# Optimization experiments

Measured on AMD Instinct MI355X. Metric: run time of the kernel, lower is better.

The kernel has to match this reference:

```python
import jax, jax.numpy as jnp
import numpy as np

ALPHA = 10.0
BETA = 2.0
BASE = 0.5
N, D, N_CLASSES = 4096, 512, 128


def setup_inputs() -> dict:
    key = jax.random.key(0)
    k1, k2 = jax.random.split(key)
    x = jax.random.normal(k1, (N, D), dtype=jnp.float32)
    inputs = x / jnp.linalg.norm(x, axis=1, keepdims=True)  # L2-normalized embeddings
    targets = jax.random.randint(k2, (N,), 0, N_CLASSES, dtype=jnp.int64)
    margin = jnp.float32(0.5)
    return {"inputs": inputs, "targets": targets, "margin": margin}


def reference(inputs, targets, margin):
    # Vectorized equivalent of the per-row masked_select/sort/hard-mining loop.
    n = inputs.shape[0]
    sim = inputs @ inputs.T  # [n, n]
    same = targets[:, None] == targets[None, :]
    pos_mask = same & (sim < 1.0)        # positives, excluding self-sim == 1
    neg_mask = ~same

    # sort()[0] / sort()[-1]  ==  masked min / max
    min_pos = jnp.min(jnp.where(pos_mask, sim, jnp.inf), axis=1)    # pos_pair_[0]
    max_neg = jnp.max(jnp.where(neg_mask, sim, -jnp.inf), axis=1)   # neg_pair_[-1]

    # Hard mining: selected values equal the raw sims (the +/- margin and
    # min_pos/max_neg shifts cancel algebraically in the original code).
    sel_neg = neg_mask & (sim + margin - min_pos[:, None] > 0)
    sel_pos = pos_mask & (max_neg[:, None] - sim + margin > 0)

    pos_sum = jnp.sum(jnp.where(sel_pos, jnp.exp(-BETA * (sim - BASE)), 0.0), axis=1)
    neg_sum = jnp.sum(jnp.where(sel_neg, jnp.exp(ALPHA * (sim - BASE)), 0.0), axis=1)
    row_loss = (2.0 / BETA) * jnp.log1p(pos_sum) + (2.0 / ALPHA) * jnp.log1p(neg_sum)

    # Rows with no surviving pos or neg pairs are skipped (counted in c).
    valid = jnp.any(sel_pos, axis=1) & jnp.any(sel_neg, axis=1)
    loss = jnp.sum(jnp.where(valid, row_loss, 0.0)) / n
    prec = jnp.mean((~valid).astype(jnp.float32))

    # Original returns mean sims of the LAST row's (pre-mining) pos/neg pairs.
    lp = pos_mask[-1].astype(sim.dtype)
    ln = neg_mask[-1].astype(sim.dtype)
    mean_pos_sim = jnp.sum(sim[-1] * lp) / jnp.maximum(jnp.sum(lp), 1.0)
    mean_neg_sim = jnp.sum(sim[-1] * ln) / jnp.maximum(jnp.sum(ln), 1.0)
    return (loss, prec, mean_pos_sim, mean_neg_sim)
```

## Files before the change

### kernel.cpp

```cpp
#include <hip/hip_runtime.h>
#include <hip/hip_bf16.h>
#include <math.h>

#define NROWS 4096
#define DDIM  512
#define BM    128
#define BK    128
#define NT    (DDIM / BK)
#define NBLK  (NROWS / BM)
#define NTRI  (NBLK * (NBLK + 1) / 2)

static constexpr float ALPHA = 10.0f;
static constexpr float BETA  = 2.0f;
static constexpr float BASE  = 0.5f;

typedef short bf16x8 __attribute__((ext_vector_type(8)));
typedef float f32x4 __attribute__((ext_vector_type(4)));

__device__ __forceinline__ unsigned f2bf(float f) {
  __hip_bfloat16 h = __float2bfloat16(f);
  return (unsigned)*reinterpret_cast<unsigned short*>(&h);
}
__device__ __forceinline__ float bf2f(unsigned short u) {
  return __uint_as_float(((unsigned)u) << 16);
}

#define GLOAD_LDS16(g, l)                                              \
  __builtin_amdgcn_global_load_lds(                                    \
      (const __attribute__((address_space(1))) void*)(g),              \
      (__attribute__((address_space(3))) void*)(l), 16, 0, 0)

__global__ __launch_bounds__(256) void convert_k(const float* __restrict__ X,
                                                 unsigned short* __restrict__ Xb) {
  const int wid = threadIdx.x >> 6, lane = threadIdx.x & 63;
  const int r = blockIdx.x * 4 + wid;
  const size_t base = (size_t)r * DDIM + lane * 8;
  const float4 v0 = *reinterpret_cast<const float4*>(X + base);
  const float4 v1 = *reinterpret_cast<const float4*>(X + base + 4);
  uint4 u;
  u.x = f2bf(v0.x) | (f2bf(v0.y) << 16);
  u.y = f2bf(v0.z) | (f2bf(v0.w) << 16);
  u.z = f2bf(v1.x) | (f2bf(v1.y) << 16);
  u.w = f2bf(v1.z) | (f2bf(v1.w) << 16);
  *reinterpret_cast<uint4*>(Xb + base) = u;
}

__global__ __launch_bounds__(256) void gemm_tri_store(
    const unsigned short* __restrict__ Xb, unsigned short* __restrict__ simb) {
  __shared__ unsigned short lds[2][BM * BK] __attribute__((aligned(16)));

  const int bswz = (blockIdx.x & 7) * (NTRI / 8) + (blockIdx.x >> 3);
  int kk0 = bswz, bi = 0;
  while (kk0 >= NBLK - bi) { kk0 -= NBLK - bi; ++bi; }
  const int bj = bi + kk0;
  const int i0 = bi * BM, j0 = bj * BM;
  const bool diagb = (bi == bj);

  const int tid = threadIdx.x;
  const int w = tid >> 6, lane = tid & 63;
  const int wr = w >> 1, wc = w & 1;
  const int g = lane >> 4, q = lane & 15;
  const char* Xbb = (const char*)Xb;

  f32x4 acc[4][4];
  #pragma unroll
  for (int m = 0; m < 4; ++m)
    #pragma unroll
    for (int n = 0; n < 4; ++n) acc[m][n] = (f32x4)0.0f;

  for (int t = 0; t < NT; ++t) {
    {
      const int kb = t * (BK * 2);
      #pragma unroll
      for (int c = 0; c < 8; ++c) {
        const int lin = (c * 256 + tid) * 16;
        const int row = lin >> 8;
        const int col = lin & 255;
        const int scol = col ^ ((row & 15) << 4);
        GLOAD_LDS16(Xbb + (size_t)(i0 + row) * (DDIM * 2) + kb + scol,
                    (char*)&lds[0][0] + lin);
        if (!diagb)
          GLOAD_LDS16(Xbb + (size_t)(j0 + row) * (DDIM * 2) + kb + scol,
                      (char*)&lds[1][0] + lin);
      }
    }
    __syncthreads();
    const char* Ab = (const char*)&lds[0][0];
    const char* Bb = diagb ? Ab : (const char*)&lds[1][0];
    #pragma unroll
    for (int kk = 0; kk < 4; ++kk) {
      bf16x8 a[4], b[4];
      #pragma unroll
      for (int fm = 0; fm < 4; ++fm) {
        const int row = wr * 64 + fm * 16 + q;
        const int colb = (kk * 64 + g * 16) ^ ((row & 15) << 4);
        a[fm] = *reinterpret_cast<const bf16x8*>(Ab + row * 256 + colb);
      }
      #pragma unroll
      for (int fn = 0; fn < 4; ++fn) {
        const int row = wc * 64 + fn * 16 + q;
        const int colb = (kk * 64 + g * 16) ^ ((row & 15) << 4);
        b[fn] = *reinterpret_cast<const bf16x8*>(Bb + row * 256 + colb);
      }
      #pragma unroll
      for (int fm = 0; fm < 4; ++fm)
        #pragma unroll
        for (int fn = 0; fn < 4; ++fn)
          acc[fm][fn] = __builtin_amdgcn_mfma_f32_16x16x32_bf16(a[fm], b[fn], acc[fm][fn], 0, 0, 0);
    }
    __syncthreads();
  }

  unsigned short* SV = &lds[0][0];

  #pragma unroll
  for (int fm = 0; fm < 4; ++fm)
    #pragma unroll
    for (int reg = 0; reg < 4; ++reg) {
      const int rloc = wr * 64 + fm * 16 + g * 4 + reg;
      #pragma unroll
      for (int fn = 0; fn < 4; ++fn) {
        const int cloc = wc * 64 + fn * 16 + q;
        unsigned short v = (unsigned short)f2bf(acc[fm][fn][reg]);
        if (diagb && rloc == cloc) v = 0x3F80;
        SV[rloc * 136 + cloc] = v;
      }
    }
  __syncthreads();
  #pragma unroll
  for (int rr = 0; rr < 8; ++rr) {
    const int s = rr * 256 + tid;
    const int row = s >> 4, cs = s & 15;
    const bf16x8 vv = *reinterpret_cast<const bf16x8*>(&SV[row * 136 + cs * 8]);
    *reinterpret_cast<bf16x8*>(simb + (size_t)(i0 + row) * NROWS + j0 + cs * 8) = vv;
  }

  if (!diagb) {
    __syncthreads();
    #pragma unroll
    for (int fn = 0; fn < 4; ++fn) {
      const int shrow = wc * 64 + fn * 16 + q;
      #pragma unroll
      for (int fm = 0; fm < 4; ++fm) {
        const int colR = wr * 64 + fm * 16 + g * 4;
        uint2 uu;
        uu.x = f2bf(acc[fm][fn][0]) | (f2bf(acc[fm][fn][1]) << 16);
        uu.y = f2bf(acc[fm][fn][2]) | (f2bf(acc[fm][fn][3]) << 16);
        *reinterpret_cast<uint2*>(&SV[shrow * 136 + colR]) = uu;
      }
    }
    __syncthreads();
    #pragma unroll
    for (int rr = 0; rr < 8; ++rr) {
      const int s = rr * 256 + tid;
      const int row = s >> 4, cs = s & 15;
      const bf16x8 vv = *reinterpret_cast<const bf16x8*>(&SV[row * 136 + cs * 8]);
      *reinterpret_cast<bf16x8*>(simb + (size_t)(j0 + row) * NROWS + i0 + cs * 8) = vv;
    }
  }
}

__global__ __launch_bounds__(256) void rows_k(
    const unsigned short* __restrict__ simb, const int* __restrict__ tgt,
    const float* __restrict__ marginp, float* __restrict__ rowloss,
    float* __restrict__ rowvalid, float* __restrict__ lacc) {
  __shared__ int tgl[NROWS];
  const int tid = threadIdx.x;
  #pragma unroll
  for (int c = 0; c < 4; ++c)
    reinterpret_cast<int4*>(tgl)[tid + c * 256] =
        reinterpret_cast<const int4*>(tgt)[tid + c * 256];
  __syncthreads();

  const int wid = tid >> 6, lane = tid & 63;
  const int i = blockIdx.x * 4 + wid;
  const int ti = tgl[i];
  const unsigned short* row = simb + (size_t)i * NROWS;
  const bool lastw = (i == NROWS - 1);

  bf16x8 v[8];
  unsigned long long same = 0ull;
  float minp = INFINITY, maxn = -INFINITY;
  #pragma unroll
  for (int c = 0; c < 8; ++c) {
    const int j0 = c * 512 + lane * 8;
    v[c] = *reinterpret_cast<const bf16x8*>(row + j0);
    const int4 t0 = *reinterpret_cast<const int4*>(tgl + j0);
    const int4 t1 = *reinterpret_cast<const int4*>(tgl + j0 + 4);
    const int tj[8] = {t0.x, t0.y, t0.z, t0.w, t1.x, t1.y, t1.z, t1.w};
    #pragma unroll
    for (int e = 0; e < 8; ++e) {
      const float s = bf2f((unsigned short)v[c][e]);
      const bool sm = (tj[e] == ti);
      same |= (unsigned long long)sm << (c * 8 + e);
      if (sm) {
        if (s < 1.0f) minp = fminf(minp, s);
      } else {
        maxn = fmaxf(maxn, s);
      }
    }
  }
  #pragma unroll
  for (int off = 1; off < 64; off <<= 1) {
    minp = fminf(minp, __shfl_xor(minp, off));
    maxn = fmaxf(maxn, __shfl_xor(maxn, off));
  }

  const float margin = *marginp;
  float psum = 0.0f, nsum = 0.0f;
  float lsp = 0.0f, lcp = 0.0f, lsn = 0.0f, lcn = 0.0f;
  #pragma unroll
  for (int c = 0; c < 8; ++c) {
    #pragma unroll
    for (int e = 0; e < 8; ++e) {
      const float s = bf2f((unsigned short)v[c][e]);
      const bool sm = (same >> (c * 8 + e)) & 1ull;
      if (!sm) {
        if (s + margin - minp > 0.0f) nsum += __expf(ALPHA * (s - BASE));
        if (lastw) { lsn += s; lcn += 1.0f; }
      } else if (s < 1.0f) {
        if (maxn - s + margin > 0.0f) psum += __expf(-BETA * (s - BASE));
        if (lastw) { lsp += s; lcp += 1.0f; }
      }
    }
  }
  #pragma unroll
  for (int off = 1; off < 64; off <<= 1) {
    psum += __shfl_xor(psum, off);
    nsum += __shfl_xor(nsum, off);
  }
  if (lastw) {
    #pragma unroll
    for (int off = 1; off < 64; off <<= 1) {
      lsp += __shfl_xor(lsp, off); lcp += __shfl_xor(lcp, off);
      lsn += __shfl_xor(lsn, off); lcn += __shfl_xor(lcn, off);
    }
  }
  if (lane == 0) {
    const bool valid = (psum > 0.0f) && (nsum > 0.0f);
    rowloss[i] = valid ? (2.0f / BETA) * log1pf(psum) + (2.0f / ALPHA) * log1pf(nsum) : 0.0f;
    rowvalid[i] = valid ? 0.0f : 1.0f;
    if (lastw) { lacc[0] = lsp; lacc[1] = lcp; lacc[2] = lsn; lacc[3] = lcn; }
  }
}

__device__ __forceinline__ float block_sum(float v) {
  __shared__ float sh[4];
  #pragma unroll
  for (int off = 32; off > 0; off >>= 1) v += __shfl_down(v, off);
  if ((threadIdx.x & 63) == 0) sh[threadIdx.x >> 6] = v;
  __syncthreads();
  float r = sh[0] + sh[1] + sh[2] + sh[3];
  __syncthreads();
  return r;
}

__global__ __launch_bounds__(256) void finalize_k(
    const float* __restrict__ rowloss, const float* __restrict__ rowvalid,
    const float* __restrict__ lacc, float* __restrict__ out) {
  float lsum = 0.0f, inval = 0.0f;
  #pragma unroll
  for (int c = 0; c < 16; ++c) {
    const int i = c * 256 + threadIdx.x;
    lsum += rowloss[i];
    inval += rowvalid[i];
  }
  lsum = block_sum(lsum);
  inval = block_sum(inval);
  if (threadIdx.x == 0) {
    out[0] = lsum / (float)NROWS;
    out[1] = inval / (float)NROWS;
    out[2] = lacc[0] / fmaxf(lacc[1], 1.0f);
    out[3] = lacc[2] / fmaxf(lacc[3], 1.0f);
  }
}

extern "C" void kernel_launch(void* const* d_in, const int* in_sizes, int n_in,
                              void* d_out, int out_size, void* d_ws, size_t ws_size,
                              hipStream_t stream) {
  const float* X = (const float*)d_in[0];
  const int* tgt = (const int*)d_in[1];
  const float* marginp = (const float*)d_in[2];
  float* out = (float*)d_out;

  char* ws = (char*)d_ws;
  float* rowloss = (float*)ws;
  float* rowvalid = (float*)(ws + (16 << 10));
  float* lacc = (float*)(ws + (32 << 10));
  unsigned short* Xb = (unsigned short*)(ws + (128 << 10));
  unsigned short* simb = (unsigned short*)(ws + (128 << 10) + ((size_t)4 << 20));

  convert_k<<<dim3(NROWS / 4), 256, 0, stream>>>(X, Xb);
  gemm_tri_store<<<dim3(NTRI), 256, 0, stream>>>(Xb, simb);
  rows_k<<<dim3(NROWS / 4), 256, 0, stream>>>(simb, tgt, marginp, rowloss, rowvalid, lacc);
  finalize_k<<<dim3(1), 256, 0, stream>>>(rowloss, rowvalid, lacc, out);
}
```

Baseline: 108.8 us.

## Double-buffer GEMM K-tiles in LDS with prefetch of next stage

Halves the K tile to 64 and allocates two LDS buffers so the global-to-LDS loads for the next K step are issued before the MFMA work on the current step. Only one barrier per iteration remains, which is meant to hide global load latency behind compute. The swizzle is adjusted to the narrower 128-byte rows. Risks include LDS bank conflicts from the weaker swizzle and more loop iterations. There is also a possible race: with no wait on the async loads before the barrier, the compute may read a buffer whose loads have not landed.

```diff
diff --git a/kernel.cpp b/kernel.cpp
--- a/kernel.cpp
+++ b/kernel.cpp
@@ -5,7 +5,7 @@
 #define NROWS 4096
 #define DDIM  512
 #define BM    128
-#define BK    128
+#define BK    64
 #define NT    (DDIM / BK)
 #define NBLK  (NROWS / BM)
 #define NTRI  (NBLK * (NBLK + 1) / 2)
@@ -47,7 +47,7 @@
 
 __global__ __launch_bounds__(256) void gemm_tri_store(
     const unsigned short* __restrict__ Xb, unsigned short* __restrict__ simb) {
-  __shared__ unsigned short lds[2][BM * BK] __attribute__((aligned(16)));
+  __shared__ unsigned short lds[2][2][BM * BK] __attribute__((aligned(16)));
 
   const int bswz = (blockIdx.x & 7) * (NTRI / 8) + (blockIdx.x >> 3);
   int kk0 = bswz, bi = 0;
@@ -68,39 +68,44 @@
     #pragma unroll
     for (int n = 0; n < 4; ++n) acc[m][n] = (f32x4)0.0f;
 
+  #define STAGE(buf, t)                                                        \
+    do {                                                                       \
+      const int kb_ = (t) * (BK * 2);                                          \
+      _Pragma("unroll")                                                        \
+      for (int c_ = 0; c_ < 4; ++c_) {                                         \
+        const int lin_ = (c_ * 256 + tid) * 16;                                \
+        const int row_ = lin_ >> 7;                                            \
+        const int col_ = lin_ & 127;                                           \
+        const int scol_ = col_ ^ ((row_ & 7) << 4);                            \
+        GLOAD_LDS16(Xbb + (size_t)(i0 + row_) * (DDIM * 2) + kb_ + scol_,      \
+                    (char*)&lds[buf][0][0] + lin_);                            \
+        if (!diagb)                                                            \
+          GLOAD_LDS16(Xbb + (size_t)(j0 + row_) * (DDIM * 2) + kb_ + scol_,    \
+                      (char*)&lds[buf][1][0] + lin_);                          \
+      }                                                                        \
+    } while (0)
+
+  STAGE(0, 0);
+  __syncthreads();
+  int cur = 0;
   for (int t = 0; t < NT; ++t) {
-    {
-      const int kb = t * (BK * 2);
-      #pragma unroll
-      for (int c = 0; c < 8; ++c) {
-        const int lin = (c * 256 + tid) * 16;
-        const int row = lin >> 8;
-        const int col = lin & 255;
-        const int scol = col ^ ((row & 15) << 4);
-        GLOAD_LDS16(Xbb + (size_t)(i0 + row) * (DDIM * 2) + kb + scol,
-                    (char*)&lds[0][0] + lin);
-        if (!diagb)
-          GLOAD_LDS16(Xbb + (size_t)(j0 + row) * (DDIM * 2) + kb + scol,
-                      (char*)&lds[1][0] + lin);
-      }
-    }
-    __syncthreads();
-    const char* Ab = (const char*)&lds[0][0];
-    const char* Bb = diagb ? Ab : (const char*)&lds[1][0];
-    #pragma unroll
-    for (int kk = 0; kk < 4; ++kk) {
+    if (t + 1 < NT) STAGE(cur ^ 1, t + 1);
+    const char* Ab = (const char*)&lds[cur][0][0];
+    const char* Bb = diagb ? Ab : (const char*)&lds[cur][1][0];
+    #pragma unroll
+    for (int kk = 0; kk < 2; ++kk) {
       bf16x8 a[4], b[4];
       #pragma unroll
       for (int fm = 0; fm < 4; ++fm) {
         const int row = wr * 64 + fm * 16 + q;
-        const int colb = (kk * 64 + g * 16) ^ ((row & 15) << 4);
-        a[fm] = *reinterpret_cast<const bf16x8*>(Ab + row * 256 + colb);
+        const int colb = (kk * 64 + g * 16) ^ ((row & 7) << 4);
+        a[fm] = *reinterpret_cast<const bf16x8*>(Ab + row * 128 + colb);
       }
       #pragma unroll
       for (int fn = 0; fn < 4; ++fn) {
         const int row = wc * 64 + fn * 16 + q;
-        const int colb = (kk * 64 + g * 16) ^ ((row & 15) << 4);
-        b[fn] = *reinterpret_cast<const bf16x8*>(Bb + row * 256 + colb);
+        const int colb = (kk * 64 + g * 16) ^ ((row & 7) << 4);
+        b[fn] = *reinterpret_cast<const bf16x8*>(Bb + row * 128 + colb);
       }
       #pragma unroll
       for (int fm = 0; fm < 4; ++fm)
@@ -109,9 +114,10 @@
           acc[fm][fn] = __builtin_amdgcn_mfma_f32_16x16x32_bf16(a[fm], b[fn], acc[fm][fn], 0, 0, 0);
     }
     __syncthreads();
-  }
-
-  unsigned short* SV = &lds[0][0];
+    cur ^= 1;
+  }
+
+  unsigned short* SV = &lds[0][0][0];
 
   #pragma unroll
   for (int fm = 0; fm < 4; ++fm)
```

After: 107.1 us. No clear change (-1.5%).
